# Optimization experiments

Measured on AMD Instinct MI355X. Metric: run time of the kernel, lower is better.

Reference implementation:

```python
import jax, jax.numpy as jnp
import numpy as np

B, N, C, H, HD, HH, WW, K, ALPHA = 8, 4096, 256, 8, 32, 64, 64, 5, 4.0


def setup_inputs() -> dict:
    key = jax.random.key(0)
    ks = jax.random.split(key, 6)
    return {
        "x": jax.random.normal(ks[0], (B, N, C), jnp.float32),
        "W_qg": jax.random.normal(ks[1], (C, 2 * C), jnp.float32) * 0.02,
        "W_kv": jax.random.normal(ks[2], (C, 2 * C), jnp.float32) * 0.02,
        "W_proj": jax.random.normal(ks[3], (C, C), jnp.float32) * 0.02,
        "b_proj": jnp.zeros((C,), jnp.float32),
        "dwc_w": jax.random.normal(ks[4], (HD, 1, K, K), jnp.float32) * 0.05,
        "dwc_b": jnp.zeros((HD,), jnp.float32),
        "power_p": jnp.zeros((1, H, 1, HD), jnp.float32),
    }


def _safe_pow(x, p):
    # x >= 0 (post-relu). 0**p == 0 for p > 0; guard base so grads stay finite.
    xs = jnp.where(x > 0, x, 1.0)
    return jnp.where(x > 0, xs ** p, 0.0)


def reference(x, W_qg, W_kv, W_proj, b_proj, dwc_w, dwc_b, power_p):
    qg = x @ W_qg                                  # (B,N,2C)
    q, g = qg[..., :C], qg[..., C:]
    kv = x @ W_kv                                  # (B,N,2C)
    k = kv[..., :C].reshape(B, N, H, HD).transpose(0, 2, 1, 3)   # (B,H,N,hd)
    v = kv[..., C:].reshape(B, N, H, HD).transpose(0, 2, 1, 3)
    q = q.reshape(B, N, H, HD).transpose(0, 2, 1, 3)

    power = 1.0 + ALPHA * jax.nn.sigmoid(power_p)  # (1,H,1,hd)
    # x_s = q_pos@kv_s + q_neg@kv_s = (q_pos+q_neg)@kv_s, kv_s = (k_pos+k_neg)^T v_s
    q_sum = _safe_pow(jax.nn.relu(q), power) + _safe_pow(jax.nn.relu(-q), power)
    k_sum = _safe_pow(jax.nn.relu(k), power) + _safe_pow(jax.nn.relu(-k), power)

    v_s, v_o = v[..., : HD // 2], v[..., HD // 2 :]
    kv_s = jnp.einsum('bhnd,bhne->bhde', k_sum, v_s)
    kv_o = jnp.einsum('bhnd,bhne->bhde', k_sum, v_o)
    x_s = jnp.einsum('bhnd,bhde->bhne', q_sum, kv_s)
    x_o = jnp.einsum('bhnd,bhde->bhne', q_sum, kv_o)
    x_att = jnp.concatenate([x_s, x_o], -1).transpose(0, 2, 1, 3).reshape(B, N, C)

    # depthwise conv branch: exact layout replication of torch permute/reshape chain
    v_img = v.transpose(0, 2, 1, 3).reshape(B * H, HD, HH, WW)
    pad = K // 2
    v_loc = jax.lax.conv_general_dilated(
        v_img, dwc_w, (1, 1), [(pad, pad), (pad, pad)],
        feature_group_count=HD,
        dimension_numbers=('NCHW', 'OIHW', 'NCHW')) + dwc_b[None, :, None, None]
    v_loc = v_loc.reshape(B, H, HD, N).transpose(0, 2, 1, 3).reshape(B, C, N).transpose(0, 2, 1)

    return ((x_att + v_loc) * g) @ W_proj + b_proj
```

## Files before the change

### kernel.cpp

```cpp
#include <hip/hip_runtime.h>
#include <hip/hip_bf16.h>
#include <math.h>

#define B_ 8
#define N_ 4096
#define C_ 256
#define H_ 8
#define HD_ 32
#define BN_ (B_ * N_)
#define E_ ((size_t)BN_ * C_)

typedef __attribute__((ext_vector_type(8))) short short8;
typedef __attribute__((ext_vector_type(4))) float f32x4;

__device__ __forceinline__ float b2f(__hip_bfloat16 x) { return __bfloat162float(x); }

__device__ __forceinline__ void gl_lds16(const void* gp, void* lp) {
    __builtin_amdgcn_global_load_lds(
        (const __attribute__((address_space(1))) unsigned int*)gp,
        (__attribute__((address_space(3))) unsigned int*)lp,
        16, 0, 0);
}

__device__ __forceinline__ float fast_abspow(float v, float p) {
    float av = fabsf(v);
    return (av > 0.f) ? __builtin_amdgcn_exp2f(p * __builtin_amdgcn_logf(av)) : 0.f;
}

__device__ __forceinline__ float bf_lo(unsigned u) { return __uint_as_float(u << 16); }
__device__ __forceinline__ float bf_hi(unsigned u) { return __uint_as_float(u & 0xffff0000u); }
__device__ __forceinline__ unsigned short f2bfbits(float f) {
    __hip_bfloat16 h = __float2bfloat16(f);
    return *(unsigned short*)&h;
}
__device__ __forceinline__ unsigned pack2(float lo, float hi) {
    return (unsigned)f2bfbits(lo) | ((unsigned)f2bfbits(hi) << 16);
}

__global__ __launch_bounds__(256) void cvt_all(
    const float* __restrict__ x, const float* __restrict__ Wqg,
    const float* __restrict__ Wkv, const float* __restrict__ Wp,
    const float* __restrict__ pp,
    __hip_bfloat16* __restrict__ xb, __hip_bfloat16* __restrict__ Wt1,
    __hip_bfloat16* __restrict__ Wt2, float* __restrict__ powers,
    float* __restrict__ kv_mat2)
{
    int t = threadIdx.x;
    int bid0 = blockIdx.x;
    if (bid0 < 4096) {
        size_t i = ((size_t)bid0 * 256 + t) * 8;
        float4 a = *(const float4*)&x[i];
        float4 b = *(const float4*)&x[i + 4];
        uint4 o = {pack2(a.x, a.y), pack2(a.z, a.w), pack2(b.x, b.y), pack2(b.z, b.w)};
        *(uint4*)&xb[i] = o;
        return;
    }
    int bid = bid0 - 4096;
    if (bid == 80) {
        powers[t] = 1.0f + 4.0f / (1.0f + expf(-pp[t]));
        return;
    }
    if (bid >= 81) {
        ((float4*)kv_mat2)[(size_t)(bid - 81) * 256 + t] = (float4){0.f, 0.f, 0.f, 0.f};
        return;
    }
    __shared__ float tile[64][65];
    const float* src;
    __hip_bfloat16* dst;
    int scols, tr, tc, dn0;
    if (bid < 32)      { src = Wqg; scols = 512; tr = bid >> 3;        tc = bid & 7;        dst = Wt1; dn0 = tc * 64; }
    else if (bid < 64) { src = Wkv; scols = 512; tr = (bid - 32) >> 3; tc = (bid - 32) & 7; dst = Wt1; dn0 = 512 + tc * 64; }
    else               { src = Wp;  scols = 256; tr = (bid - 64) >> 2; tc = (bid - 64) & 3; dst = Wt2; dn0 = tc * 64; }
    int tx = t & 63, ty = t >> 6;
    #pragma unroll
    for (int i = 0; i < 16; i++) {
        int r = ty + i * 4;
        tile[r][tx] = src[(size_t)(tr * 64 + r) * scols + tc * 64 + tx];
    }
    __syncthreads();
    #pragma unroll
    for (int i = 0; i < 16; i++) {
        int n_local = ty + i * 4;
        dst[(size_t)(dn0 + n_local) * 256 + tr * 64 + tx] = __float2bfloat16(tile[tx][n_local]);
    }
}

__global__ __launch_bounds__(256) void gemm1_mfma(
    const __hip_bfloat16* __restrict__ xb, const __hip_bfloat16* __restrict__ Wt1,
    const float* __restrict__ powers,
    __hip_bfloat16* __restrict__ q16, __hip_bfloat16* __restrict__ k16,
    __hip_bfloat16* __restrict__ g16, __hip_bfloat16* __restrict__ v16)
{
    __shared__ __align__(16) unsigned short ABs[128 * 128];
    unsigned short* As = ABs;
    unsigned short* Bs = ABs + 128 * 64;
    int t = threadIdx.x;
    int w = t >> 6, l = t & 63;
    int bswz = (blockIdx.x & 7) * 256 + (blockIdx.x >> 3);
    int row0 = (bswz >> 3) * 128;
    int colb = bswz & 7;
    int col0 = colb * 128;
    int wm = (w >> 1) * 64, wn = (w & 1) * 64;
    int lane15 = l & 15, quad = l >> 4;
    int sr8 = l >> 3;
    int sc = ((l & 7) ^ sr8) * 8;
    int r7 = lane15 & 7;

    f32x4 acc[4][4];
    #pragma unroll
    for (int mi = 0; mi < 4; mi++)
        #pragma unroll
        for (int ni = 0; ni < 4; ni++) acc[mi][ni] = (f32x4){0.f, 0.f, 0.f, 0.f};

    for (int k0 = 0; k0 < 256; k0 += 64) {
        #pragma unroll
        for (int j = 0; j < 4; j++) {
            int rowl = j * 32 + w * 8 + sr8;
            gl_lds16(&xb[(size_t)(row0 + rowl) * 256 + k0 + sc],
                     &As[(j * 32 + w * 8) * 64]);
            gl_lds16(&Wt1[(size_t)(col0 + rowl) * 256 + k0 + sc],
                     &Bs[(j * 32 + w * 8) * 64]);
        }
        __syncthreads();
        #pragma unroll
        for (int kh = 0; kh < 2; kh++) {
            int cs_k = ((kh * 4 + quad) ^ r7) * 8;
            short8 a[4], b[4];
            #pragma unroll
            for (int mi = 0; mi < 4; mi++)
                a[mi] = *(const short8*)&As[(wm + mi * 16 + lane15) * 64 + cs_k];
            #pragma unroll
            for (int ni = 0; ni < 4; ni++)
                b[ni] = *(const short8*)&Bs[(wn + ni * 16 + lane15) * 64 + cs_k];
            #pragma unroll
            for (int mi = 0; mi < 4; mi++)
                #pragma unroll
                for (int ni = 0; ni < 4; ni++)
                    acc[mi][ni] = __builtin_amdgcn_mfma_f32_16x16x32_bf16(a[mi], b[ni], acc[mi][ni], 0, 0, 0);
        }
        __syncthreads();
    }

    int region = colb >> 1;
    bool dopow = (region == 0) || (region == 2);
    __hip_bfloat16* dst = (region == 0) ? q16 : (region == 1) ? g16 : (region == 2) ? k16 : v16;
    int cbase = col0 & 255;
    #pragma unroll
    for (int mi = 0; mi < 4; mi++) {
        #pragma unroll
        for (int ni = 0; ni < 4; ni++) {
            int rowb = wm + mi * 16 + quad * 4;
            int coll = wn + ni * 16 + lane15;
            float p = powers[cbase + coll];
            int cchunk = coll >> 3, cin = coll & 7;
            #pragma unroll
            for (int r = 0; r < 4; r++) {
                int rl = rowb + r;
                float v = acc[mi][ni][r];
                float o = dopow ? fast_abspow(v, p) : v;
                ABs[rl * 128 + ((cchunk ^ (rl & 15)) << 3) + cin] = f2bfbits(o);
            }
        }
    }
    __syncthreads();
    #pragma unroll
    for (int j = 0; j < 8; j++) {
        int g = j * 256 + t;
        int rl = g >> 4, chunk = g & 15;
        uint4 vv = *(const uint4*)&ABs[rl * 128 + ((chunk ^ (rl & 15)) << 3)];
        *(uint4*)&dst[(size_t)(row0 + rl) * 256 + cbase + chunk * 8] = vv;
    }
}

__global__ __launch_bounds__(256) void kvconv_kernel(
    const __hip_bfloat16* __restrict__ k16, const __hip_bfloat16* __restrict__ v16,
    float* __restrict__ kv_mat2,
    const float* __restrict__ w, const float* __restrict__ bias,
    __hip_bfloat16* __restrict__ vloc)
{
    __shared__ __align__(16) unsigned char smraw[18560];
    int t = threadIdx.x;

    if (blockIdx.x < 512) {
        unsigned short (*KV)[32][136] = (unsigned short (*)[32][136])smraw;
        int w_ = t >> 6, l = t & 63;
        int lane15 = l & 15, quad = l >> 4;
        int bid = blockIdx.x;
        int pair = bid >> 3, seg = bid & 7;
        int b = pair >> 3, h = pair & 7;
        int nloc = t & 127, cs = (t >> 7) * 16;

        f32x4 acc[2][2];
        #pragma unroll
        for (int di = 0; di < 2; di++)
            #pragma unroll
            for (int ei = 0; ei < 2; ei++) acc[di][ei] = (f32x4){0.f, 0.f, 0.f, 0.f};

        const size_t base = (size_t)b * N_ * 256 + h * 32 + cs;
        for (int c4 = 0; c4 < 4; c4++) {
            int n0 = seg * 512 + c4 * 128;
            const uint4* kp = (const uint4*)(k16 + base + (size_t)(n0 + nloc) * 256);
            uint4 ka = kp[0], kb = kp[1];
            const uint4* vp = (const uint4*)(v16 + base + (size_t)(n0 + nloc) * 256);
            uint4 va = vp[0], vb = vp[1];
            __syncthreads();
            unsigned kw[8] = {ka.x, ka.y, ka.z, ka.w, kb.x, kb.y, kb.z, kb.w};
            unsigned vw[8] = {va.x, va.y, va.z, va.w, vb.x, vb.y, vb.z, vb.w};
            #pragma unroll
            for (int j = 0; j < 8; j++) {
                KV[0][cs + 2 * j][nloc]     = (unsigned short)(kw[j] & 0xffffu);
                KV[0][cs + 2 * j + 1][nloc] = (unsigned short)(kw[j] >> 16);
                KV[1][cs + 2 * j][nloc]     = (unsigned short)(vw[j] & 0xffffu);
                KV[1][cs + 2 * j + 1][nloc] = (unsigned short)(vw[j] >> 16);
            }
            __syncthreads();
            int nb = w_ * 32 + quad * 8;
            short8 a[2], bb[2];
            #pragma unroll
            for (int di = 0; di < 2; di++)
                a[di] = *(const short8*)&KV[0][di * 16 + lane15][nb];
            #pragma unroll
            for (int ei = 0; ei < 2; ei++)
                bb[ei] = *(const short8*)&KV[1][ei * 16 + lane15][nb];
            #pragma unroll
            for (int di = 0; di < 2; di++)
                #pragma unroll
                for (int ei = 0; ei < 2; ei++)
                    acc[di][ei] = __builtin_amdgcn_mfma_f32_16x16x32_bf16(a[di], bb[ei], acc[di][ei], 0, 0, 0);
        }

        __syncthreads();
        float* red = (float*)smraw;
        #pragma unroll
        for (int di = 0; di < 2; di++)
            #pragma unroll
            for (int ei = 0; ei < 2; ei++) {
                int e = ei * 16 + lane15;
                #pragma unroll
                for (int r = 0; r < 4; r++) {
                    int d = di * 16 + quad * 4 + r;
                    red[w_ * 1056 + e * 33 + d] = acc[di][ei][r];
                }
            }
        __syncthreads();
        #pragma unroll
        for (int j = 0; j < 4; j++) {
            int o = j * 256 + t;
            int e = o >> 5, d = o & 31;
            float s = red[e * 33 + d] + red[1056 + e * 33 + d]
                    + red[2112 + e * 33 + d] + red[3168 + e * 33 + d];
            atomicAdd(&kv_mat2[(size_t)b * 8192 + e * 256 + h * 32 + d], s);
        }
        return;
    }

    float* img = (float*)smraw;
    float* wl  = (float*)(smraw + 18432);
    int gid = blockIdx.x - 512;
    int DD = gid & 31;
    if (t < 128) {
        int row = t >> 1, side = (t & 1) * 68;
        *(float4*)&img[row * 72 + side] = (float4){0.f, 0.f, 0.f, 0.f};
    }
    if (t < 25) wl[t] = w[DD * 25 + t];
    {
        int row = t >> 2, colb = (t & 3) * 16;
        const uint4* src = (const uint4*)(v16 + (size_t)gid * 4096 + row * 64 + colb);
        uint4 u0 = src[0], u1 = src[1];
        float4* d = (float4*)&img[row * 72 + 4 + colb];
        d[0] = (float4){bf_lo(u0.x), bf_hi(u0.x), bf_lo(u0.y), bf_hi(u0.y)};
        d[1] = (float4){bf_lo(u0.z), bf_hi(u0.z), bf_lo(u0.w), bf_hi(u0.w)};
        d[2] = (float4){bf_lo(u1.x), bf_hi(u1.x), bf_lo(u1.y), bf_hi(u1.y)};
        d[3] = (float4){bf_lo(u1.z), bf_hi(u1.z), bf_lo(u1.w), bf_hi(u1.w)};
    }
    __syncthreads();
    float bs = bias[DD];
    int x0 = (t & 15) * 4, yb = t >> 4;
    #pragma unroll
    for (int s = 0; s < 4; s++) {
        int y = yb + s * 16;
        float a0 = bs, a1 = bs, a2 = bs, a3 = bs;
        #pragma unroll
        for (int ky = 0; ky < 5; ky++) {
            int row = y + ky - 2;
            if (row < 0 || row >= 64) continue;
            const float* rp = &img[row * 72 + x0];
            float4 w0 = *(const float4*)rp;
            float4 w1 = *(const float4*)(rp + 4);
            float4 w2 = *(const float4*)(rp + 8);
            float win[12] = {w0.x, w0.y, w0.z, w0.w, w1.x, w1.y, w1.z, w1.w,
                             w2.x, w2.y, w2.z, w2.w};
            #pragma unroll
            for (int kx = 0; kx < 5; kx++) {
                float wt = wl[ky * 5 + kx];
                a0 += wt * win[2 + kx];
                a1 += wt * win[3 + kx];
                a2 += wt * win[4 + kx];
                a3 += wt * win[5 + kx];
            }
        }
        unsigned lo = pack2(a0, a1);
        unsigned hi = pack2(a2, a3);
        *(uint2*)(vloc + (size_t)gid * 4096 + y * 64 + x0) = (uint2){lo, hi};
    }
}

#define A2P 264
__global__ __launch_bounds__(256) void att_gemm2(
    const __hip_bfloat16* __restrict__ q16, const float* __restrict__ kv_mat2,
    const __hip_bfloat16* __restrict__ vloc, const __hip_bfloat16* __restrict__ g16,
    const __hip_bfloat16* __restrict__ Wt2, const float* __restrict__ bp,
    float* __restrict__ out)
{
    __shared__ __align__(16) unsigned short QA[64 * A2P];
    __shared__ __align__(16) unsigned short Bs[256 * 64];
    int t = threadIdx.x;
    int w = t >> 6, l = t & 63;
    int r0 = blockIdx.x * 64;
    int b = r0 >> 12, n0 = r0 & 4095;
    int lane15 = l & 15, quad = l >> 4;
    int h0 = w * 2;
    int sr8 = l >> 3;
    int sc = ((l & 7) ^ sr8) * 8;
    int r7 = lane15 & 7;

    {
        const uint4* qsrc = (const uint4*)(q16 + (size_t)(r0 + (t >> 2)) * 256 + (t & 3) * 64);
        uint4* qdst = (uint4*)&QA[(t >> 2) * A2P + (t & 3) * 64];
        #pragma unroll
        for (int j = 0; j < 8; j++) qdst[j] = qsrc[j];
    }
    __syncthreads();

    short8 afr[4][2];
    #pragma unroll
    for (int m = 0; m < 4; m++)
        #pragma unroll
        for (int hh = 0; hh < 2; hh++)
            afr[m][hh] = *(const short8*)&QA[(m * 16 + lane15) * A2P + (h0 + hh) * 32 + quad * 8];

    short8 bfr[2][2];
    #pragma unroll
    for (int hh = 0; hh < 2; hh++) {
        #pragma unroll
        for (int nt = 0; nt < 2; nt++) {
            const float4* kp = (const float4*)(kv_mat2 + (size_t)b * 8192 +
                (size_t)(nt * 16 + lane15) * 256 + (h0 + hh) * 32 + quad * 8);
            float4 ka = kp[0], kb = kp[1];
            short8 bb;
            bb[0] = (short)f2bfbits(ka.x); bb[1] = (short)f2bfbits(ka.y);
            bb[2] = (short)f2bfbits(ka.z); bb[3] = (short)f2bfbits(ka.w);
            bb[4] = (short)f2bfbits(kb.x); bb[5] = (short)f2bfbits(kb.y);
            bb[6] = (short)f2bfbits(kb.z); bb[7] = (short)f2bfbits(kb.w);
            bfr[hh][nt] = bb;
        }
    }

    f32x4 ac[4][2][2];
    #pragma unroll
    for (int m = 0; m < 4; m++)
        #pragma unroll
        for (int hh = 0; hh < 2; hh++)
            #pragma unroll
            for (int nt = 0; nt < 2; nt++)
                ac[m][hh][nt] = __builtin_amdgcn_mfma_f32_16x16x32_bf16(
                    afr[m][hh], bfr[hh][nt], (f32x4){0.f, 0.f, 0.f, 0.f}, 0, 0, 0);

    #pragma unroll
    for (int m = 0; m < 4; m++) {
        #pragma unroll
        for (int hh = 0; hh < 2; hh++) {
            #pragma unroll
            for (int nt = 0; nt < 2; nt++) {
                int col = (h0 + hh) * 32 + nt * 16 + lane15;
                int rowb = m * 16 + quad * 4;
                size_t img = ((size_t)((b * 8 + (col & 7)) * 32 + (col >> 3))) * 4096 + n0 + rowb;
                uint2 vv = *(const uint2*)(vloc + img);
                float vl[4] = {bf_lo(vv.x), bf_hi(vv.x), bf_lo(vv.y), bf_hi(vv.y)};
                #pragma unroll
                for (int i = 0; i < 4; i++) {
                    float gg = b2f(g16[(size_t)(r0 + rowb + i) * 256 + col]);
                    float val = (ac[m][hh][nt][i] + vl[i]) * gg;
                    QA[(rowb + i) * A2P + col] = f2bfbits(val);
                }
            }
        }
    }

    int wm = (w & 1) * 32, wn = (w >> 1) * 128;
    f32x4 acc2[2][8];
    #pragma unroll
    for (int mi = 0; mi < 2; mi++)
        #pragma unroll
        for (int ni = 0; ni < 8; ni++) acc2[mi][ni] = (f32x4){0.f, 0.f, 0.f, 0.f};

    for (int k0 = 0; k0 < 256; k0 += 64) {
        __syncthreads();
        #pragma unroll
        for (int j = 0; j < 8; j++) {
            int rowl = j * 32 + w * 8 + sr8;
            gl_lds16(&Wt2[(size_t)rowl * 256 + k0 + sc],
                     &Bs[(j * 32 + w * 8) * 64]);
        }
        __syncthreads();
        #pragma unroll
        for (int h2 = 0; h2 < 2; h2++) {
            int cs_k = ((h2 * 4 + quad) ^ r7) * 8;
            short8 a[2], bb[8];
            #pragma unroll
            for (int mi = 0; mi < 2; mi++)
                a[mi] = *(const short8*)&QA[(wm + mi * 16 + lane15) * A2P + k0 + h2 * 32 + quad * 8];
            #pragma unroll
            for (int ni = 0; ni < 8; ni++)
                bb[ni] = *(const short8*)&Bs[(wn + ni * 16 + lane15) * 64 + cs_k];
            #pragma unroll
            for (int mi = 0; mi < 2; mi++)
                #pragma unroll
                for (int ni = 0; ni < 8; ni++)
                    acc2[mi][ni] = __builtin_amdgcn_mfma_f32_16x16x32_bf16(a[mi], bb[ni], acc2[mi][ni], 0, 0, 0);
        }
    }

    #pragma unroll
    for (int mi = 0; mi < 2; mi++) {
        #pragma unroll
        for (int ni = 0; ni < 8; ni++) {
            int row = r0 + wm + mi * 16 + quad * 4;
            int col = wn + ni * 16 + lane15;
            float bv = bp[col];
            #pragma unroll
            for (int r = 0; r < 4; r++)
                out[(size_t)(row + r) * 256 + col] = acc2[mi][ni][r] + bv;
        }
    }
}

extern "C" void kernel_launch(void* const* d_in, const int* in_sizes, int n_in,
                              void* d_out, int out_size, void* d_ws, size_t ws_size,
                              hipStream_t stream) {
    const float* x      = (const float*)d_in[0];
    const float* W_qg   = (const float*)d_in[1];
    const float* W_kv   = (const float*)d_in[2];
    const float* W_proj = (const float*)d_in[3];
    const float* b_proj = (const float*)d_in[4];
    const float* dwc_w  = (const float*)d_in[5];
    const float* dwc_b  = (const float*)d_in[6];
    const float* pow_p  = (const float*)d_in[7];
    float* out = (float*)d_out;

    float* ws = (float*)d_ws;
    const size_t E = E_;
    __hip_bfloat16* q16  = (__hip_bfloat16*)ws;
    __hip_bfloat16* k16  = (__hip_bfloat16*)(ws + E / 2);
    __hip_bfloat16* g16  = (__hip_bfloat16*)(ws + E);
    __hip_bfloat16* v16  = (__hip_bfloat16*)(ws + 3 * E / 2);
    __hip_bfloat16* xb   = (__hip_bfloat16*)(ws + 2 * E);
    __hip_bfloat16* vl16 = (__hip_bfloat16*)(ws + 5 * E / 2);
    float* kv_mat2 = ws + 3 * E;
    __hip_bfloat16* Wt1 = (__hip_bfloat16*)(kv_mat2 + 65536);
    __hip_bfloat16* Wt2 = Wt1 + 262144;
    float* powers = (float*)(Wt2 + 65536);

    cvt_all<<<4096 + 81 + 64, 256, 0, stream>>>(x, W_qg, W_kv, W_proj, pow_p, xb, Wt1, Wt2, powers, kv_mat2);
    gemm1_mfma<<<2048, 256, 0, stream>>>(xb, Wt1, powers, q16, k16, g16, v16);
    kvconv_kernel<<<512 + 2048, 256, 0, stream>>>(k16, v16, kv_mat2, dwc_w, dwc_b, vl16);
    att_gemm2<<<512, 256, 0, stream>>>(q16, kv_mat2, vl16, g16, Wt2, b_proj, out);
}
```

Baseline: 171.1 us.

## Split gemm1 into k/v pass and fuse q/g GEMM with kv-reduction and conv

The first projection GEMM is split so that only the k and v columns are computed up front. The q and g columns are computed inside a merged kernel alongside the kv-matrix reduction and the depthwise conv blocks, so those independent workloads can overlap on the GPU. Separately, the final GEMM epilogue stages its fp32 output through LDS and writes it back as coalesced float4 rows instead of scattered scalar stores. The merged kernel's LDS footprint grows to 32KB, which may reduce occupancy for the conv and reduction blocks.

```diff
diff --git a/kernel.cpp b/kernel.cpp
--- a/kernel.cpp
+++ b/kernel.cpp
@@ -35,6 +35,83 @@
 }
 __device__ __forceinline__ unsigned pack2(float lo, float hi) {
     return (unsigned)f2bfbits(lo) | ((unsigned)f2bfbits(hi) << 16);
+}
+
+__device__ __forceinline__ void gemm1_body(
+    unsigned short* ABs, int t, int row0, int col0, bool dopow,
+    const __hip_bfloat16* __restrict__ xb, const __hip_bfloat16* __restrict__ Wt1,
+    const float* __restrict__ powers, __hip_bfloat16* __restrict__ dst)
+{
+    unsigned short* As = ABs;
+    unsigned short* Bs = ABs + 128 * 64;
+    int w = t >> 6, l = t & 63;
+    int wm = (w >> 1) * 64, wn = (w & 1) * 64;
+    int lane15 = l & 15, quad = l >> 4;
+    int sr8 = l >> 3;
+    int sc = ((l & 7) ^ sr8) * 8;
+    int r7 = lane15 & 7;
+
+    f32x4 acc[4][4];
+    #pragma unroll
+    for (int mi = 0; mi < 4; mi++)
+        #pragma unroll
+        for (int ni = 0; ni < 4; ni++) acc[mi][ni] = (f32x4){0.f, 0.f, 0.f, 0.f};
+
+    for (int k0 = 0; k0 < 256; k0 += 64) {
+        #pragma unroll
+        for (int j = 0; j < 4; j++) {
+            int rowl = j * 32 + w * 8 + sr8;
+            gl_lds16(&xb[(size_t)(row0 + rowl) * 256 + k0 + sc],
+                     &As[(j * 32 + w * 8) * 64]);
+            gl_lds16(&Wt1[(size_t)(col0 + rowl) * 256 + k0 + sc],
+                     &Bs[(j * 32 + w * 8) * 64]);
+        }
+        __syncthreads();
+        #pragma unroll
+        for (int kh = 0; kh < 2; kh++) {
+            int cs_k = ((kh * 4 + quad) ^ r7) * 8;
+            short8 a[4], b[4];
+            #pragma unroll
+            for (int mi = 0; mi < 4; mi++)
+                a[mi] = *(const short8*)&As[(wm + mi * 16 + lane15) * 64 + cs_k];
+            #pragma unroll
+            for (int ni = 0; ni < 4; ni++)
+                b[ni] = *(const short8*)&Bs[(wn + ni * 16 + lane15) * 64 + cs_k];
+            #pragma unroll
+            for (int mi = 0; mi < 4; mi++)
+                #pragma unroll
+                for (int ni = 0; ni < 4; ni++)
+                    acc[mi][ni] = __builtin_amdgcn_mfma_f32_16x16x32_bf16(a[mi], b[ni], acc[mi][ni], 0, 0, 0);
+        }
+        __syncthreads();
+    }
+
+    int cbase = col0 & 255;
+    #pragma unroll
+    for (int mi = 0; mi < 4; mi++) {
+        #pragma unroll
+        for (int ni = 0; ni < 4; ni++) {
+            int rowb = wm + mi * 16 + quad * 4;
+            int coll = wn + ni * 16 + lane15;
+            float p = powers[cbase + coll];
+            int cchunk = coll >> 3, cin = coll & 7;
+            #pragma unroll
+            for (int r = 0; r < 4; r++) {
+                int rl = rowb + r;
+                float v = acc[mi][ni][r];
+                float o = dopow ? fast_abspow(v, p) : v;
+                ABs[rl * 128 + ((cchunk ^ (rl & 15)) << 3) + cin] = f2bfbits(o);
+            }
+        }
+    }
+    __syncthreads();
+    #pragma unroll
+    for (int j = 0; j < 8; j++) {
+        int g = j * 256 + t;
+        int rl = g >> 4, chunk = g & 15;
+        uint4 vv = *(const uint4*)&ABs[rl * 128 + ((chunk ^ (rl & 15)) << 3)];
+        *(uint4*)&dst[(size_t)(row0 + rl) * 256 + cbase + chunk * 8] = vv;
+    }
 }
 
 __global__ __launch_bounds__(256) void cvt_all(
@@ -85,107 +162,51 @@
     }
 }
 
-__global__ __launch_bounds__(256) void gemm1_mfma(
+__global__ __launch_bounds__(256) void gemm1_kv(
     const __hip_bfloat16* __restrict__ xb, const __hip_bfloat16* __restrict__ Wt1,
     const float* __restrict__ powers,
-    __hip_bfloat16* __restrict__ q16, __hip_bfloat16* __restrict__ k16,
-    __hip_bfloat16* __restrict__ g16, __hip_bfloat16* __restrict__ v16)
+    __hip_bfloat16* __restrict__ k16, __hip_bfloat16* __restrict__ v16)
 {
     __shared__ __align__(16) unsigned short ABs[128 * 128];
-    unsigned short* As = ABs;
-    unsigned short* Bs = ABs + 128 * 64;
     int t = threadIdx.x;
-    int w = t >> 6, l = t & 63;
-    int bswz = (blockIdx.x & 7) * 256 + (blockIdx.x >> 3);
-    int row0 = (bswz >> 3) * 128;
-    int colb = bswz & 7;
-    int col0 = colb * 128;
-    int wm = (w >> 1) * 64, wn = (w & 1) * 64;
-    int lane15 = l & 15, quad = l >> 4;
-    int sr8 = l >> 3;
-    int sc = ((l & 7) ^ sr8) * 8;
-    int r7 = lane15 & 7;
-
-    f32x4 acc[4][4];
-    #pragma unroll
-    for (int mi = 0; mi < 4; mi++)
-        #pragma unroll
-        for (int ni = 0; ni < 4; ni++) acc[mi][ni] = (f32x4){0.f, 0.f, 0.f, 0.f};
-
-    for (int k0 = 0; k0 < 256; k0 += 64) {
-        #pragma unroll
-        for (int j = 0; j < 4; j++) {
-            int rowl = j * 32 + w * 8 + sr8;
-            gl_lds16(&xb[(size_t)(row0 + rowl) * 256 + k0 + sc],
-                     &As[(j * 32 + w * 8) * 64]);
-            gl_lds16(&Wt1[(size_t)(col0 + rowl) * 256 + k0 + sc],
-                     &Bs[(j * 32 + w * 8) * 64]);
-        }
-        __syncthreads();
-        #pragma unroll
-        for (int kh = 0; kh < 2; kh++) {
-            int cs_k = ((kh * 4 + quad) ^ r7) * 8;
-            short8 a[4], b[4];
-            #pragma unroll
-            for (int mi = 0; mi < 4; mi++)
-                a[mi] = *(const short8*)&As[(wm + mi * 16 + lane15) * 64 + cs_k];
-            #pragma unroll
-            for (int ni = 0; ni < 4; ni++)
-                b[ni] = *(const short8*)&Bs[(wn + ni * 16 + lane15) * 64 + cs_k];
-            #pragma unroll
-            for (int mi = 0; mi < 4; mi++)
-                #pragma unroll
-                for (int ni = 0; ni < 4; ni++)
-                    acc[mi][ni] = __builtin_amdgcn_mfma_f32_16x16x32_bf16(a[mi], b[ni], acc[mi][ni], 0, 0, 0);
-        }
-        __syncthreads();
-    }
-
-    int region = colb >> 1;
-    bool dopow = (region == 0) || (region == 2);
-    __hip_bfloat16* dst = (region == 0) ? q16 : (region == 1) ? g16 : (region == 2) ? k16 : v16;
-    int cbase = col0 & 255;
-    #pragma unroll
-    for (int mi = 0; mi < 4; mi++) {
-        #pragma unroll
-        for (int ni = 0; ni < 4; ni++) {
-            int rowb = wm + mi * 16 + quad * 4;
-            int coll = wn + ni * 16 + lane15;
-            float p = powers[cbase + coll];
-            int cchunk = coll >> 3, cin = coll & 7;
-            #pragma unroll
-            for (int r = 0; r < 4; r++) {
-                int rl = rowb + r;
-                float v = acc[mi][ni][r];
-                float o = dopow ? fast_abspow(v, p) : v;
-                ABs[rl * 128 + ((cchunk ^ (rl & 15)) << 3) + cin] = f2bfbits(o);
-            }
-        }
-    }
-    __syncthreads();
-    #pragma unroll
-    for (int j = 0; j < 8; j++) {
-        int g = j * 256 + t;
-        int rl = g >> 4, chunk = g & 15;
-        uint4 vv = *(const uint4*)&ABs[rl * 128 + ((chunk ^ (rl & 15)) << 3)];
-        *(uint4*)&dst[(size_t)(row0 + rl) * 256 + cbase + chunk * 8] = vv;
-    }
-}
-
-__global__ __launch_bounds__(256) void kvconv_kernel(
+    int bswz = (blockIdx.x & 7) * 128 + (blockIdx.x >> 3);
+    int row0 = (bswz >> 2) * 128;
+    int c2 = bswz & 3;
+    int col0 = 512 + c2 * 128;
+    bool dopow = (c2 < 2);
+    __hip_bfloat16* dst = (c2 < 2) ? k16 : v16;
+    gemm1_body(ABs, t, row0, col0, dopow, xb, Wt1, powers, dst);
+}
+
+__global__ __launch_bounds__(256) void mega_kernel(
+    const __hip_bfloat16* __restrict__ xb, const __hip_bfloat16* __restrict__ Wt1,
+    const float* __restrict__ powers,
+    __hip_bfloat16* __restrict__ q16, __hip_bfloat16* __restrict__ g16,
     const __hip_bfloat16* __restrict__ k16, const __hip_bfloat16* __restrict__ v16,
     float* __restrict__ kv_mat2,
     const float* __restrict__ w, const float* __restrict__ bias,
     __hip_bfloat16* __restrict__ vloc)
 {
-    __shared__ __align__(16) unsigned char smraw[18560];
+    __shared__ __align__(16) unsigned char smraw[32768];
     int t = threadIdx.x;
 
-    if (blockIdx.x < 512) {
+    if (blockIdx.x < 1024) {
+        int bid = blockIdx.x;
+        int bswz = (bid & 7) * 128 + (bid >> 3);
+        int row0 = (bswz >> 2) * 128;
+        int c2 = bswz & 3;
+        int col0 = c2 * 128;
+        bool dopow = (c2 < 2);
+        __hip_bfloat16* dst = (c2 < 2) ? q16 : g16;
+        gemm1_body((unsigned short*)smraw, t, row0, col0, dopow, xb, Wt1, powers, dst);
+        return;
+    }
+
+    if (blockIdx.x < 1536) {
         unsigned short (*KV)[32][136] = (unsigned short (*)[32][136])smraw;
         int w_ = t >> 6, l = t & 63;
         int lane15 = l & 15, quad = l >> 4;
-        int bid = blockIdx.x;
+        int bid = blockIdx.x - 1024;
         int pair = bid >> 3, seg = bid & 7;
         int b = pair >> 3, h = pair & 7;
         int nloc = t & 127, cs = (t >> 7) * 16;
@@ -256,7 +277,7 @@
 
     float* img = (float*)smraw;
     float* wl  = (float*)(smraw + 18432);
-    int gid = blockIdx.x - 512;
+    int gid = blockIdx.x - 1536;
     int DD = gid & 31;
     if (t < 128) {
         int row = t >> 1, side = (t & 1) * 68;
@@ -312,8 +333,9 @@
     const __hip_bfloat16* __restrict__ Wt2, const float* __restrict__ bp,
     float* __restrict__ out)
 {
-    __shared__ __align__(16) unsigned short QA[64 * A2P];
-    __shared__ __align__(16) unsigned short Bs[256 * 64];
+    __shared__ __align__(16) unsigned char sm2[66560];
+    unsigned short* QA = (unsigned short*)sm2;
+    unsigned short* Bs = (unsigned short*)(sm2 + 64 * A2P * 2);
     int t = threadIdx.x;
     int w = t >> 6, l = t & 63;
     int r0 = blockIdx.x * 64;
@@ -421,17 +443,26 @@
         }
     }
 
+    __syncthreads();
+    float* outs = (float*)sm2;
     #pragma unroll
     for (int mi = 0; mi < 2; mi++) {
         #pragma unroll
         for (int ni = 0; ni < 8; ni++) {
-            int row = r0 + wm + mi * 16 + quad * 4;
+            int rowl = wm + mi * 16 + quad * 4;
             int col = wn + ni * 16 + lane15;
             float bv = bp[col];
             #pragma unroll
             for (int r = 0; r < 4; r++)
-                out[(size_t)(row + r) * 256 + col] = acc2[mi][ni][r] + bv;
-        }
+                outs[(rowl + r) * 260 + col] = acc2[mi][ni][r] + bv;
+        }
+    }
+    __syncthreads();
+    int orow = t >> 2, oc0 = (t & 3) * 64;
+    #pragma unroll
+    for (int j = 0; j < 16; j++) {
+        float4 v4 = *(const float4*)&outs[orow * 260 + oc0 + j * 4];
+        *(float4*)&out[(size_t)(r0 + orow) * 256 + oc0 + j * 4] = v4;
     }
 }
 
@@ -462,7 +493,7 @@
     float* powers = (float*)(Wt2 + 65536);
 
     cvt_all<<<4096 + 81 + 64, 256, 0, stream>>>(x, W_qg, W_kv, W_proj, pow_p, xb, Wt1, Wt2, powers, kv_mat2);
-    gemm1_mfma<<<2048, 256, 0, stream>>>(xb, Wt1, powers, q16, k16, g16, v16);
-    kvconv_kernel<<<512 + 2048, 256, 0, stream>>>(k16, v16, kv_mat2, dwc_w, dwc_b, vl16);
+    gemm1_kv<<<1024, 256, 0, stream>>>(xb, Wt1, powers, k16, v16);
+    mega_kernel<<<3584, 256, 0, stream>>>(xb, Wt1, powers, q16, g16, k16, v16, kv_mat2, dwc_w, dwc_b, vl16);
     att_gemm2<<<512, 256, 0, stream>>>(q16, kv_mat2, vl16, g16, Wt2, b_proj, out);
 }
```

Result: slower. 199.5 us (+16.6%).
